# Optimization experiments

Hardware: AMD Instinct MI355X
Metric: run time of the kernel (lower is better)

## Reference

```python
import jax, jax.numpy as jnp
import numpy as np

GROUP_SIZE = 32
OUT_FEATURES = 4096
IN_FEATURES = 4096
NUM_GROUPS = OUT_FEATURES * IN_FEATURES // GROUP_SIZE  # 524288
PACKED_SIZE = (GROUP_SIZE + 1) // 2  # 16


def setup_inputs() -> dict:
    key = jax.random.key(0)
    k1, k2, k3, k4 = jax.random.split(key, 4)
    x = jax.random.normal(k1, (8, 2048, IN_FEATURES), dtype=jnp.float32)
    # two 3-bit values per byte -> valid packed values are in [0, 64)
    weight_packed = jax.random.randint(k2, (NUM_GROUPS, PACKED_SIZE), 0, 64, dtype=jnp.int32)
    weight_scales = jax.random.uniform(k3, (NUM_GROUPS,), minval=0.01, maxval=1.0).astype(jnp.float16)
    bias = jax.random.normal(k4, (OUT_FEATURES,)).astype(jnp.float16)
    return {"x": x, "weight_packed": weight_packed, "weight_scales": weight_scales, "bias": bias}


def _dequantize(weight_packed, weight_scales):
    # unpack: even positions = low 3 bits, odd positions = bits 3..5
    low = weight_packed & 7          # [G, P]
    high = (weight_packed >> 3) & 7  # [G, P]
    q = jnp.stack([low, high], axis=-1).reshape(NUM_GROUPS, GROUP_SIZE)  # interleaved [G, 32]
    # dequant: q/7 in [0,1] -> [-1,1] -> * per-group scale
    w = (q.astype(jnp.float32) * (2.0 / 7.0) - 1.0) * weight_scales.astype(jnp.float32)[:, None]
    return w.reshape(OUT_FEATURES, IN_FEATURES)


def reference(x, weight_packed, weight_scales, bias):
    W = _dequantize(weight_packed, weight_scales)  # [out, in] fp32
    # F.linear: x @ W.T + b
    return jnp.einsum('bsi,oi->bso', x, W) + bias.astype(jnp.float32)
```

## Files before the change

### kernel.cpp

```cpp
#include <hip/hip_runtime.h>


#define K_DIM 4096
#define N_DIM 4096

#define BM 128
#define BN 128
#define BK 64

#define BM2 256
#define BN2 256
#define BK2 64
#define NT2 (K_DIM / BK2)

typedef __bf16 bf16_t;
typedef __bf16 bf16x8 __attribute__((ext_vector_type(8)));
typedef float f32x4 __attribute__((ext_vector_type(4)));

__device__ __forceinline__ void gload16(const void* g, void* l) {
    __builtin_amdgcn_global_load_lds(
        (const __attribute__((address_space(1))) unsigned int*)g,
        (__attribute__((address_space(3))) unsigned int*)l, 16, 0, 0);
}

__global__ __launch_bounds__(256) void dequant_kernel(const int4* __restrict__ wp4,
                                                      const float* __restrict__ scales,
                                                      bf16x8* __restrict__ W) {
    const int t = blockIdx.x * 256 + threadIdx.x;
    const int4 p = wp4[t];
    const float s = scales[t >> 2];
    const float c = 2.0f / 7.0f;
    int v[4] = {p.x, p.y, p.z, p.w};
    bf16x8 o;
#pragma unroll
    for (int i = 0; i < 4; ++i) {
        float w0 = fmaf((float)(v[i] & 7), c, -1.0f) * s;
        float w1 = fmaf((float)((v[i] >> 3) & 7), c, -1.0f) * s;
        o[2 * i]     = (__bf16)w0;
        o[2 * i + 1] = (__bf16)w1;
    }
    W[t] = o;
}

__global__ __launch_bounds__(256) void convx_kernel(const float4* __restrict__ X4,
                                                    bf16x8* __restrict__ Xb) {
    const int t = blockIdx.x * 256 + threadIdx.x;
    float4 a = X4[2 * t];
    float4 b = X4[2 * t + 1];
    bf16x8 o;
    o[0] = (__bf16)a.x; o[1] = (__bf16)a.y; o[2] = (__bf16)a.z; o[3] = (__bf16)a.w;
    o[4] = (__bf16)b.x; o[5] = (__bf16)b.y; o[6] = (__bf16)b.z; o[7] = (__bf16)b.w;
    Xb[t] = o;
}

__global__ __launch_bounds__(512, 2) void gemm256_kernel(const bf16_t* __restrict__ A,
                                                         const bf16_t* __restrict__ B,
                                                         const float* __restrict__ bias,
                                                         float* __restrict__ C) {
    __shared__ __align__(16) bf16_t As[2][BM2 * BK2];
    __shared__ __align__(16) bf16_t Bs[2][BN2 * BK2];

    const int tid  = threadIdx.x;
    const int lane = tid & 63;
    const int wv   = tid >> 6;
    const int wm   = (wv >> 2) * 128;
    const int wn   = (wv & 3) * 64;

    const int nwg = gridDim.x;
    const int bid = blockIdx.x;
    const int swz = (bid & 7) * (nwg >> 3) + (bid >> 3);
    const int n0  = (swz & 15) * BN2;
    const int m0  = (swz >> 4) * BM2;

    f32x4 acc[8][4];
#pragma unroll
    for (int i = 0; i < 8; ++i)
#pragma unroll
        for (int j = 0; j < 4; ++j) acc[i][j] = {0.f, 0.f, 0.f, 0.f};

    const int r8  = lane >> 3;
    const int csw = ((lane & 7) ^ r8) << 3;
    const bf16_t* aSrc = A + (size_t)(m0 + wv * 8 + r8) * K_DIM + csw;
    const bf16_t* bSrc = B + (size_t)(n0 + wv * 8 + r8) * K_DIM + csw;

    auto stage = [&](int buf, int k0) {
#pragma unroll
        for (int r = 0; r < 4; ++r) {
            gload16(aSrc + (size_t)(r * 64) * K_DIM + k0, &As[buf][(r * 64 + wv * 8) * BK2]);
            gload16(bSrc + (size_t)(r * 64) * K_DIM + k0, &Bs[buf][(r * 64 + wv * 8) * BK2]);
        }
    };

    const int mrow = lane & 15;
    const int quad = lane >> 4;
    const int m7   = mrow & 7;
    const int sw0  = ((quad ^ m7) << 3);
    const int sw1  = (((quad + 4) ^ m7) << 3);
    const int offA0 = (wm + mrow) * BK2 + sw0;
    const int offA1 = (wm + mrow) * BK2 + sw1;
    const int offB0 = (wn + mrow) * BK2 + sw0;
    const int offB1 = (wn + mrow) * BK2 + sw1;

    stage(0, 0);
    stage(1, BK2);

    for (int t = 0; t < NT2; ++t) {
        const int cur = t & 1;
        if (t < NT2 - 1) {
            asm volatile("s_waitcnt vmcnt(8)" ::: "memory");
        } else {
            asm volatile("s_waitcnt vmcnt(0)" ::: "memory");
        }
        __builtin_amdgcn_s_barrier();
        asm volatile("" ::: "memory");

        const bf16_t* as = &As[cur][0];
        const bf16_t* bs = &Bs[cur][0];

        bf16x8 a0[8], b0[4];
#pragma unroll
        for (int i = 0; i < 8; ++i) a0[i] = *(const bf16x8*)(as + offA0 + i * (16 * BK2));
#pragma unroll
        for (int j = 0; j < 4; ++j) b0[j] = *(const bf16x8*)(bs + offB0 + j * (16 * BK2));
        __builtin_amdgcn_s_setprio(1);
#pragma unroll
        for (int i = 0; i < 8; ++i)
#pragma unroll
            for (int j = 0; j < 4; ++j)
                acc[i][j] = __builtin_amdgcn_mfma_f32_16x16x32_bf16(a0[i], b0[j],
                                                                    acc[i][j], 0, 0, 0);
        __builtin_amdgcn_s_setprio(0);

        bf16x8 a1[8], b1[4];
#pragma unroll
        for (int i = 0; i < 8; ++i) a1[i] = *(const bf16x8*)(as + offA1 + i * (16 * BK2));
#pragma unroll
        for (int j = 0; j < 4; ++j) b1[j] = *(const bf16x8*)(bs + offB1 + j * (16 * BK2));
        __builtin_amdgcn_s_setprio(1);
#pragma unroll
        for (int i = 0; i < 8; ++i)
#pragma unroll
            for (int j = 0; j < 4; ++j)
                acc[i][j] = __builtin_amdgcn_mfma_f32_16x16x32_bf16(a1[i], b1[j],
                                                                    acc[i][j], 0, 0, 0);
        __builtin_amdgcn_s_setprio(0);

        asm volatile("" ::: "memory");
        __builtin_amdgcn_s_barrier();
        asm volatile("" ::: "memory");
        if (t + 2 < NT2) stage(cur, (t + 2) * BK2);
    }

    const int col   = lane & 15;
    const int rbase = (lane >> 4) * 4;
#pragma unroll
    for (int j = 0; j < 4; ++j) {
        const int n  = n0 + wn + j * 16 + col;
        const float bn = bias[n];
#pragma unroll
        for (int i = 0; i < 8; ++i) {
            const size_t base = (size_t)(m0 + wm + i * 16 + rbase) * N_DIM + n;
#pragma unroll
            for (int r = 0; r < 4; ++r)
                C[base + (size_t)r * N_DIM] = acc[i][j][r] + bn;
        }
    }
}

template <bool PRE>
__global__ __launch_bounds__(256) void gemm_kernel(const void* __restrict__ Ap,
                                                   const bf16_t* __restrict__ B,
                                                   const float* __restrict__ bias,
                                                   float* __restrict__ C) {
    __shared__ __align__(16) bf16_t As[BM * BK];
    __shared__ __align__(16) bf16_t Bs[BN * BK];

    const int tid  = threadIdx.x;
    const int lane = tid & 63;
    const int wv   = tid >> 6;
    const int wm   = (wv & 1) * 64;
    const int wn   = (wv >> 1) * 64;
    const int m0   = blockIdx.y * BM;
    const int n0   = blockIdx.x * BN;

    f32x4 acc[4][4];
#pragma unroll
    for (int i = 0; i < 4; ++i)
#pragma unroll
        for (int j = 0; j < 4; ++j) acc[i][j] = {0.f, 0.f, 0.f, 0.f};

    const int r8   = lane >> 3;
    const int kc   = (lane & 7) * 8;
    const int mrow = lane & 15;
    const int quad = lane >> 4;

    for (int k0 = 0; k0 < K_DIM; k0 += BK) {
        __syncthreads();
        if (PRE) {
            const bf16_t* A = (const bf16_t*)Ap;
#pragma unroll
            for (int c = 0; c < 4; ++c) {
                const int rowb = wv * 32 + c * 8;
                gload16(A + (size_t)(m0 + rowb + r8) * K_DIM + k0 + kc, &As[rowb * BK]);
                gload16(B + (size_t)(n0 + rowb + r8) * K_DIM + k0 + kc, &Bs[rowb * BK]);
            }
        } else {
            const float* A = (const float*)Ap;
            const int row = tid >> 1;
            const int kh  = (tid & 1) * 32;
            const float4* ga = (const float4*)(A + (size_t)(m0 + row) * K_DIM + k0 + kh);
            bf16x8* dst = (bf16x8*)&As[row * BK + kh];
#pragma unroll
            for (int c = 0; c < 4; ++c) {
                float4 u = ga[2 * c];
                float4 v = ga[2 * c + 1];
                bf16x8 o;
                o[0] = (__bf16)u.x; o[1] = (__bf16)u.y; o[2] = (__bf16)u.z; o[3] = (__bf16)u.w;
                o[4] = (__bf16)v.x; o[5] = (__bf16)v.y; o[6] = (__bf16)v.z; o[7] = (__bf16)v.w;
                dst[c] = o;
            }
#pragma unroll
            for (int c = 0; c < 4; ++c) {
                const int rowb = wv * 32 + c * 8;
                gload16(B + (size_t)(n0 + rowb + r8) * K_DIM + k0 + kc, &Bs[rowb * BK]);
            }
        }
        __syncthreads();

#pragma unroll
        for (int kk = 0; kk < BK; kk += 32) {
            bf16x8 af[4], bfr[4];
#pragma unroll
            for (int i = 0; i < 4; ++i)
                af[i] = *(const bf16x8*)&As[(wm + i * 16 + mrow) * BK + kk + quad * 8];
#pragma unroll
            for (int j = 0; j < 4; ++j)
                bfr[j] = *(const bf16x8*)&Bs[(wn + j * 16 + mrow) * BK + kk + quad * 8];
#pragma unroll
            for (int i = 0; i < 4; ++i)
#pragma unroll
                for (int j = 0; j < 4; ++j)
                    acc[i][j] = __builtin_amdgcn_mfma_f32_16x16x32_bf16(af[i], bfr[j],
                                                                        acc[i][j], 0, 0, 0);
        }
    }

    const int col   = lane & 15;
    const int rbase = (lane >> 4) * 4;
#pragma unroll
    for (int j = 0; j < 4; ++j) {
        const int n  = n0 + wn + j * 16 + col;
        const float bn = bias[n];
#pragma unroll
        for (int i = 0; i < 4; ++i) {
            const size_t base = (size_t)(m0 + wm + i * 16 + rbase) * N_DIM + n;
#pragma unroll
            for (int r = 0; r < 4; ++r)
                C[base + (size_t)r * N_DIM] = acc[i][j][r] + bn;
        }
    }
}

extern "C" void kernel_launch(void* const* d_in, const int* in_sizes, int n_in,
                              void* d_out, int out_size, void* d_ws, size_t ws_size,
                              hipStream_t stream) {
    const float* x      = (const float*)d_in[0];
    const int*   wp     = (const int*)d_in[1];
    const float* scales = (const float*)d_in[2];
    const float* bias   = (const float*)d_in[3];
    float*       out    = (float*)d_out;

    const int M = in_sizes[0] / K_DIM;

    bf16_t* Wb = (bf16_t*)d_ws;
    const size_t wbytes = (size_t)N_DIM * K_DIM * sizeof(bf16_t);
    bf16_t* Xb = (bf16_t*)((char*)d_ws + wbytes);
    const size_t need = wbytes + (size_t)M * K_DIM * sizeof(bf16_t);

    dequant_kernel<<<(N_DIM * K_DIM / 8) / 256, 256, 0, stream>>>(
        (const int4*)wp, scales, (bf16x8*)Wb);

    if (ws_size >= need && (M % BM2) == 0) {
        convx_kernel<<<((size_t)M * K_DIM / 8) / 256, 256, 0, stream>>>(
            (const float4*)x, (bf16x8*)Xb);
        dim3 grid2((unsigned)((M / BM2) * (N_DIM / BN2)));
        gemm256_kernel<<<grid2, 512, 0, stream>>>(Xb, Wb, bias, out);
    } else {
        dim3 grid(N_DIM / BN, M / BM);
        gemm_kernel<false><<<grid, 256, 0, stream>>>(x, Wb, bias, out);
    }
}
```

Measured before the change: 1.070 ms.

## Split GEMM K-tile into half-slabs with interleaved A/B prefetch per quarter

Restructures the 256x256 bf16 GEMM main loop to use four 32-wide K half-slabs in LDS instead of two 64-wide buffers. Global-to-LDS loads for A and B are issued separately between four MFMA phases, each phase guarded by barriers, so prefetch is spread more finely across the compute. The LDS swizzle and load mapping change to match the 32-wide rows. This adds more barriers per iteration and depends on a delicate vmcnt/slot-reuse ordering, which carries a correctness risk.

```diff
diff --git a/kernel.cpp b/kernel.cpp
--- a/kernel.cpp
+++ b/kernel.cpp
@@ -22,6 +22,8 @@
         (const __attribute__((address_space(1))) unsigned int*)g,
         (__attribute__((address_space(3))) unsigned int*)l, 16, 0, 0);
 }
+
+#define MFMA16(a, b, c) __builtin_amdgcn_mfma_f32_16x16x32_bf16((a), (b), (c), 0, 0, 0)
 
 __global__ __launch_bounds__(256) void dequant_kernel(const int4* __restrict__ wp4,
                                                       const float* __restrict__ scales,
@@ -57,8 +59,8 @@
                                                          const bf16_t* __restrict__ B,
                                                          const float* __restrict__ bias,
                                                          float* __restrict__ C) {
-    __shared__ __align__(16) bf16_t As[2][BM2 * BK2];
-    __shared__ __align__(16) bf16_t Bs[2][BN2 * BK2];
+    __shared__ __align__(16) bf16_t As[4][BM2 * 32];
+    __shared__ __align__(16) bf16_t Bs[4][BN2 * 32];
 
     const int tid  = threadIdx.x;
     const int lane = tid & 63;
@@ -68,9 +70,9 @@
 
     const int nwg = gridDim.x;
     const int bid = blockIdx.x;
-    const int swz = (bid & 7) * (nwg >> 3) + (bid >> 3);
-    const int n0  = (swz & 15) * BN2;
-    const int m0  = (swz >> 4) * BM2;
+    const int swzb = (bid & 7) * (nwg >> 3) + (bid >> 3);
+    const int n0  = (swzb & 15) * BN2;
+    const int m0  = (swzb >> 4) * BM2;
 
     f32x4 acc[8][4];
 #pragma unroll
@@ -78,78 +80,102 @@
 #pragma unroll
         for (int j = 0; j < 4; ++j) acc[i][j] = {0.f, 0.f, 0.f, 0.f};
 
-    const int r8  = lane >> 3;
-    const int csw = ((lane & 7) ^ r8) << 3;
-    const bf16_t* aSrc = A + (size_t)(m0 + wv * 8 + r8) * K_DIM + csw;
-    const bf16_t* bSrc = B + (size_t)(n0 + wv * 8 + r8) * K_DIM + csw;
-
-    auto stage = [&](int buf, int k0) {
-#pragma unroll
-        for (int r = 0; r < 4; ++r) {
-            gload16(aSrc + (size_t)(r * 64) * K_DIM + k0, &As[buf][(r * 64 + wv * 8) * BK2]);
-            gload16(bSrc + (size_t)(r * 64) * K_DIM + k0, &Bs[buf][(r * 64 + wv * 8) * BK2]);
-        }
-    };
+    const int l4  = lane >> 2;
+    const int gsw = ((lane & 3) ^ ((lane >> 3) & 3)) * 8;
+    const bf16_t* aSrc = A + (size_t)(m0 + wv * 16 + l4) * K_DIM + gsw;
+    const bf16_t* bSrc = B + (size_t)(n0 + wv * 16 + l4) * K_DIM + gsw;
+    const int ldsOff = wv * 512;
 
     const int mrow = lane & 15;
     const int quad = lane >> 4;
-    const int m7   = mrow & 7;
-    const int sw0  = ((quad ^ m7) << 3);
-    const int sw1  = (((quad + 4) ^ m7) << 3);
-    const int offA0 = (wm + mrow) * BK2 + sw0;
-    const int offA1 = (wm + mrow) * BK2 + sw1;
-    const int offB0 = (wn + mrow) * BK2 + sw0;
-    const int offB1 = (wn + mrow) * BK2 + sw1;
-
-    stage(0, 0);
-    stage(1, BK2);
+    const int sq   = (quad ^ ((mrow >> 1) & 3)) * 8;
+    const int offA = (wm + mrow) * 32 + sq;
+    const int offB = (wn + mrow) * 32 + sq;
+
+#define STAGE_A(slot, kb)                                               \
+    do {                                                                \
+        gload16(aSrc + (kb), &As[slot][ldsOff]);                        \
+        gload16(aSrc + (size_t)128 * K_DIM + (kb), &As[slot][4096 + ldsOff]); \
+    } while (0)
+#define STAGE_B(slot, kb)                                               \
+    do {                                                                \
+        gload16(bSrc + (kb), &Bs[slot][ldsOff]);                        \
+        gload16(bSrc + (size_t)128 * K_DIM + (kb), &Bs[slot][4096 + ldsOff]); \
+    } while (0)
+
+    STAGE_A(0, 0);  STAGE_B(0, 0);
+    STAGE_A(1, 32); STAGE_B(1, 32);
+    STAGE_A(2, 64); STAGE_B(2, 64);
+    asm volatile("s_waitcnt vmcnt(4)" ::: "memory");
+    __builtin_amdgcn_s_barrier();
 
     for (int t = 0; t < NT2; ++t) {
         const int cur = t & 1;
-        if (t < NT2 - 1) {
-            asm volatile("s_waitcnt vmcnt(8)" ::: "memory");
-        } else {
-            asm volatile("s_waitcnt vmcnt(0)" ::: "memory");
-        }
-        __builtin_amdgcn_s_barrier();
-        asm volatile("" ::: "memory");
-
-        const bf16_t* as = &As[cur][0];
-        const bf16_t* bs = &Bs[cur][0];
-
-        bf16x8 a0[8], b0[4];
-#pragma unroll
-        for (int i = 0; i < 8; ++i) a0[i] = *(const bf16x8*)(as + offA0 + i * (16 * BK2));
-#pragma unroll
-        for (int j = 0; j < 4; ++j) b0[j] = *(const bf16x8*)(bs + offB0 + j * (16 * BK2));
+        const int sA0 = cur * 2;
+        const int sA1 = cur * 2 + 1;
+        const int sN1 = (cur ^ 1) * 2 + 1;
+        const int kb1 = (t + 1) * BK2 + 32;
+        const int kb2 = (t + 2) * BK2;
+        const bool st1 = (t + 1) < NT2;
+        const bool st2 = (t + 2) < NT2;
+
+        bf16x8 a[4], b[4];
+
+#pragma unroll
+        for (int i = 0; i < 4; ++i) a[i] = *(const bf16x8*)&As[sA0][offA + i * 512];
+#pragma unroll
+        for (int j = 0; j < 4; ++j) b[j] = *(const bf16x8*)&Bs[sA0][offB + j * 512];
+        if (st1) STAGE_A(sN1, kb1);
+        __builtin_amdgcn_s_barrier();
         __builtin_amdgcn_s_setprio(1);
 #pragma unroll
-        for (int i = 0; i < 8; ++i)
-#pragma unroll
-            for (int j = 0; j < 4; ++j)
-                acc[i][j] = __builtin_amdgcn_mfma_f32_16x16x32_bf16(a0[i], b0[j],
-                                                                    acc[i][j], 0, 0, 0);
+        for (int i = 0; i < 4; ++i)
+#pragma unroll
+            for (int j = 0; j < 4; ++j) acc[i][j] = MFMA16(a[i], b[j], acc[i][j]);
         __builtin_amdgcn_s_setprio(0);
-
-        bf16x8 a1[8], b1[4];
-#pragma unroll
-        for (int i = 0; i < 8; ++i) a1[i] = *(const bf16x8*)(as + offA1 + i * (16 * BK2));
-#pragma unroll
-        for (int j = 0; j < 4; ++j) b1[j] = *(const bf16x8*)(bs + offB1 + j * (16 * BK2));
+        __builtin_amdgcn_s_barrier();
+
+#pragma unroll
+        for (int i = 0; i < 4; ++i) a[i] = *(const bf16x8*)&As[sA0][offA + (i + 4) * 512];
+        if (st1) STAGE_B(sN1, kb1);
+        __builtin_amdgcn_s_barrier();
         __builtin_amdgcn_s_setprio(1);
 #pragma unroll
-        for (int i = 0; i < 8; ++i)
-#pragma unroll
-            for (int j = 0; j < 4; ++j)
-                acc[i][j] = __builtin_amdgcn_mfma_f32_16x16x32_bf16(a1[i], b1[j],
-                                                                    acc[i][j], 0, 0, 0);
+        for (int i = 0; i < 4; ++i)
+#pragma unroll
+            for (int j = 0; j < 4; ++j) acc[i + 4][j] = MFMA16(a[i], b[j], acc[i + 4][j]);
         __builtin_amdgcn_s_setprio(0);
-
-        asm volatile("" ::: "memory");
-        __builtin_amdgcn_s_barrier();
-        asm volatile("" ::: "memory");
-        if (t + 2 < NT2) stage(cur, (t + 2) * BK2);
-    }
+        __builtin_amdgcn_s_barrier();
+
+#pragma unroll
+        for (int i = 0; i < 4; ++i) a[i] = *(const bf16x8*)&As[sA1][offA + i * 512];
+#pragma unroll
+        for (int j = 0; j < 4; ++j) b[j] = *(const bf16x8*)&Bs[sA1][offB + j * 512];
+        if (st2) STAGE_A(sA0, kb2);
+        __builtin_amdgcn_s_barrier();
+        __builtin_amdgcn_s_setprio(1);
+#pragma unroll
+        for (int i = 0; i < 4; ++i)
+#pragma unroll
+            for (int j = 0; j < 4; ++j) acc[i][j] = MFMA16(a[i], b[j], acc[i][j]);
+        __builtin_amdgcn_s_setprio(0);
+        __builtin_amdgcn_s_barrier();
+
+#pragma unroll
+        for (int i = 0; i < 4; ++i) a[i] = *(const bf16x8*)&As[sA1][offA + (i + 4) * 512];
+        if (st2) STAGE_B(sA0, kb2);
+        asm volatile("s_waitcnt vmcnt(4)" ::: "memory");
+        __builtin_amdgcn_s_barrier();
+        __builtin_amdgcn_s_setprio(1);
+#pragma unroll
+        for (int i = 0; i < 4; ++i)
+#pragma unroll
+            for (int j = 0; j < 4; ++j) acc[i + 4][j] = MFMA16(a[i], b[j], acc[i + 4][j]);
+        __builtin_amdgcn_s_setprio(0);
+        __builtin_amdgcn_s_barrier();
+    }
+#undef STAGE_A
+#undef STAGE_B
 
     const int col   = lane & 15;
     const int rbase = (lane >> 4) * 4;
```

Measured after the change: 1.019 ms. 1.05x faster.
